# Kernel tuning notes

Measured on AMD Instinct MI355X. Metric: run time of the kernel, lower is better.

## Reference

```python
import jax, jax.numpy as jnp
import numpy as np

N, E = 50000, 800000
F_IN, F_OUT, H = 128, 16, 8
NEG_SLOPE = 0.2  # PyG GATConv default
EPS = 1e-5       # LayerNorm eps


def setup_inputs() -> dict:
    key = jax.random.key(0)
    ks = jax.random.split(key, 8)
    x = jax.random.normal(ks[0], (N, F_IN), dtype=jnp.float32)
    edge_index = jax.random.randint(ks[1], (2, E), 0, N, dtype=jnp.int32)
    s_in = 1.0 / np.sqrt(F_IN)
    s_f = 1.0 / np.sqrt(F_OUT)
    W = jax.random.normal(ks[2], (F_IN, H * F_OUT), dtype=jnp.float32) * s_in
    att_src = jax.random.normal(ks[3], (H, F_OUT), dtype=jnp.float32) * s_f
    att_dst = jax.random.normal(ks[4], (H, F_OUT), dtype=jnp.float32) * s_f
    bias = jnp.zeros((H * F_OUT,), dtype=jnp.float32)
    gamma = jnp.ones((H * F_OUT,), dtype=jnp.float32)
    beta = jnp.zeros((H * F_OUT,), dtype=jnp.float32)
    return {"x": x, "edge_index": edge_index, "W": W, "att_src": att_src,
            "att_dst": att_dst, "bias": bias, "gamma": gamma, "beta": beta}


def _gat_layer(x, edge_index, W, att_src, att_dst, bias, gamma, beta):
    n = x.shape[0]
    # add self loops (PyG GATConv default add_self_loops=True)
    loop = jnp.arange(n, dtype=edge_index.dtype)
    src = jnp.concatenate([edge_index[0], loop])  # message source j
    dst = jnp.concatenate([edge_index[1], loop])  # message target i

    xp = (x @ W).reshape(n, H, F_OUT)                      # [N,H,F]
    a_src = jnp.einsum('nhf,hf->nh', xp, att_src)          # [N,H]
    a_dst = jnp.einsum('nhf,hf->nh', xp, att_dst)          # [N,H]

    e = a_src[src] + a_dst[dst]                            # [E+N,H]
    e = jax.nn.leaky_relu(e, NEG_SLOPE)
    # softmax over incoming edges per destination node
    m = jax.ops.segment_max(e, dst, num_segments=n)        # [N,H]
    e = jnp.exp(e - m[dst])
    z = jax.ops.segment_sum(e, dst, num_segments=n)        # [N,H]
    alpha = e / jnp.where(z[dst] > 0, z[dst], 1.0)         # [E+N,H]

    msg = alpha[:, :, None] * xp[src]                      # [E+N,H,F]
    out = jax.ops.segment_sum(msg, dst, num_segments=n)    # [N,H,F]
    out = out.reshape(n, H * F_OUT) + bias

    # LayerNorm over feature dim
    mu = out.mean(axis=-1, keepdims=True)
    var = out.var(axis=-1, keepdims=True)
    return (out - mu) * jax.lax.rsqrt(var + EPS) * gamma + beta


def reference(x, edge_index, W, att_src, att_dst, bias, gamma, beta):
    return _gat_layer(x, edge_index, W, att_src, att_dst, bias, gamma, beta)
```

## Files before the change

### kernel.cpp

```cpp
#include <hip/hip_runtime.h>
#include <math.h>

#define F_IN 128
#define NHD 8
#define FEAT 128
#define NEG_SLOPE 0.2f
#define LN_EPS 1e-5f
#define BSH 7
#define BMSK 127
#define NPQ 16
#define CAP 48
#define EPB 4096
#define NBMAX 512
#define BCAP 6144
#define WCOLS 144

typedef __bf16 v8bf __attribute__((ext_vector_type(8)));
typedef __bf16 v4bf __attribute__((ext_vector_type(4)));
typedef __bf16 v2bf __attribute__((ext_vector_type(2)));
typedef float f32x4 __attribute__((ext_vector_type(4)));

__global__ __launch_bounds__(256) void k_wt(const float* __restrict__ W,
                                            const float* __restrict__ att_src,
                                            const float* __restrict__ att_dst,
                                            __bf16* __restrict__ WT,
                                            int* __restrict__ gcnt, int NB) {
    int idx = blockIdx.x * 256 + threadIdx.x;
    if (idx < NB) gcnt[idx] = 0;
    int c = idx >> 7, k = idx & 127;
    float v;
    if (c < 128) {
        v = W[k * 128 + c];
    } else if (c < 136) {
        int h = c - 128;
        float s = 0.f;
#pragma unroll
        for (int f = 0; f < 16; ++f) s += W[k * 128 + h * 16 + f] * att_src[h * 16 + f];
        v = s;
    } else {
        int h = c - 136;
        float s = 0.f;
#pragma unroll
        for (int f = 0; f < 16; ++f) s += W[k * 128 + h * 16 + f] * att_dst[h * 16 + f];
        v = s;
    }
    WT[c * 128 + k] = (__bf16)v;
}

__global__ __launch_bounds__(512) void k_fused(const float* __restrict__ x,
                                               const __bf16* __restrict__ WT,
                                               __bf16* __restrict__ xp16,
                                               float* __restrict__ a_src,
                                               float* __restrict__ a_dst,
                                               const int* __restrict__ src,
                                               const int* __restrict__ dst,
                                               unsigned int* __restrict__ sorted2,
                                               int* __restrict__ gcnt,
                                               int n, int E, int Ga) {
    __shared__ __align__(16) char smem[34816];
    if ((int)blockIdx.x < Ga) {
        unsigned int* sorted_l = (unsigned int*)smem;
        int* lcnt = (int*)(smem + 16384);
        int* loff = (int*)(smem + 16384 + 2048);
        int* wtot = (int*)(smem + 16384 + 2048 + 2052);
        int* wexcl = (int*)(smem + 16384 + 2048 + 2052 + 32);
        int* goff = (int*)(smem + 16384 + 2048 + 2052 + 64);
        int NB = (n + BMSK) >> BSH;
        int tid = threadIdx.x, lane = tid & 63, wid = tid >> 6;
        long base0 = (long)blockIdx.x * EPB;
        long total = (long)E + n;
        if (tid < NB) lcnt[tid] = 0;
        __syncthreads();

        int s0[8], d0[8];
        bool val[8];
        long e0 = base0 + (long)tid * 8;
        if (e0 + 7 < E) {
            int4 sa = *(const int4*)(src + e0);
            int4 sb = *(const int4*)(src + e0 + 4);
            int4 da = *(const int4*)(dst + e0);
            int4 db = *(const int4*)(dst + e0 + 4);
            s0[0] = sa.x; s0[1] = sa.y; s0[2] = sa.z; s0[3] = sa.w;
            s0[4] = sb.x; s0[5] = sb.y; s0[6] = sb.z; s0[7] = sb.w;
            d0[0] = da.x; d0[1] = da.y; d0[2] = da.z; d0[3] = da.w;
            d0[4] = db.x; d0[5] = db.y; d0[6] = db.z; d0[7] = db.w;
#pragma unroll
            for (int j = 0; j < 8; ++j) val[j] = true;
        } else {
#pragma unroll
            for (int j = 0; j < 8; ++j) {
                long e = e0 + j;
                val[j] = (e < total);
                s0[j] = d0[j] = 0;
                if (val[j]) {
                    if (e < E) { s0[j] = src[e]; d0[j] = dst[e]; }
                    else { s0[j] = d0[j] = (int)(e - E); }
                }
            }
        }
#pragma unroll
        for (int j = 0; j < 8; ++j)
            if (val[j]) atomicAdd(&lcnt[d0[j] >> BSH], 1);
        __syncthreads();

        int v = (tid < NB) ? lcnt[tid] : 0;
        int xx = v;
#pragma unroll
        for (int o = 1; o < 64; o <<= 1) {
            int t2 = __shfl_up(xx, o);
            if (lane >= o) xx += t2;
        }
        if (lane == 63) wtot[wid] = xx;
        __syncthreads();
        if (wid == 0 && lane < 8) {
            int s = wtot[lane];
            int y = s;
#pragma unroll
            for (int o = 1; o < 8; o <<= 1) {
                int t2 = __shfl_up(y, o);
                if (lane >= o) y += t2;
            }
            wexcl[lane] = y - s;
        }
        __syncthreads();
        int excl = wexcl[wid] + xx - v;
        if (tid < NB) loff[tid] = excl;
        if (tid == NB - 1) loff[NB] = excl + v;
        __syncthreads();
        if (tid < NB) lcnt[tid] = loff[tid];
        __syncthreads();
#pragma unroll
        for (int j = 0; j < 8; ++j) {
            if (val[j]) {
                int b = d0[j] >> BSH;
                int pos = atomicAdd(&lcnt[b], 1);
                sorted_l[pos] = ((unsigned)b << 23) | ((unsigned)s0[j] << 7) |
                                (unsigned)(d0[j] & BMSK);
            }
        }
        __syncthreads();
        if (tid < NB) {
            int len = loff[tid + 1] - loff[tid];
            goff[tid] = (len > 0) ? atomicAdd(&gcnt[tid], len) : 0;
        }
        __syncthreads();
        int tv = loff[NB];
        for (int i = tid; i < tv; i += 512) {
            unsigned int u = sorted_l[i];
            int b = (int)(u >> 23);
            int r = goff[b] + (i - loff[b]);
            if (r < BCAP)
                sorted2[(long)b * BCAP + r] = u & 0x7FFFFFu;
        }
    } else {
        __bf16 (*xs)[136] = (__bf16 (*)[136])smem;
        __bf16 (*ot)[136] = (__bf16 (*)[136])(smem + 17408);
        int gb = blockIdx.x - Ga;
        int tid = threadIdx.x;
        int rowbase = gb * 64;
        {
            int i4 = tid;
#pragma unroll
            for (int rep = 0; rep < 4; ++rep, i4 += 512) {
                int r = i4 >> 5, c4 = i4 & 31;
                int gr = rowbase + r; if (gr > n - 1) gr = n - 1;
                float4 xv = *(const float4*)(x + (long)gr * 128 + c4 * 4);
                v4bf pk;
                pk[0] = (__bf16)xv.x; pk[1] = (__bf16)xv.y;
                pk[2] = (__bf16)xv.z; pk[3] = (__bf16)xv.w;
                *(v4bf*)(&xs[r][c4 * 4]) = pk;
            }
        }
        __syncthreads();
        int wv = tid >> 6;
        int lane = tid & 63;
        int m = lane & 15, quad = lane >> 4;
        int colbase = wv * 16;
        const __bf16* wcol = WT + (colbase + m) * 128;
        v8bf wf[4];
#pragma unroll
        for (int kk = 0; kk < 4; ++kk)
            wf[kk] = *(const v8bf*)(wcol + kk * 32 + quad * 8);
        v8bf wf2[4];
        if (wv < 4) {
            const __bf16* wcol2 = WT + (128 + m) * 128;
#pragma unroll
            for (int kk = 0; kk < 4; ++kk)
                wf2[kk] = *(const v8bf*)(wcol2 + kk * 32 + quad * 8);
        }
#pragma unroll
        for (int t = 0; t < 4; ++t) {
            int rb = t * 16;
            f32x4 acc = {0.f, 0.f, 0.f, 0.f};
#pragma unroll
            for (int kk = 0; kk < 4; ++kk) {
                v8bf a = *(const v8bf*)(&xs[rb + m][kk * 32 + quad * 8]);
                acc = __builtin_amdgcn_mfma_f32_16x16x32_bf16(a, wf[kk], acc, 0, 0, 0);
            }
#pragma unroll
            for (int r = 0; r < 4; ++r)
                ot[rb + quad * 4 + r][colbase + m] = (__bf16)acc[r];
        }
        if (wv < 4) {
            int rb = wv * 16;
            f32x4 acc = {0.f, 0.f, 0.f, 0.f};
#pragma unroll
            for (int kk = 0; kk < 4; ++kk) {
                v8bf a = *(const v8bf*)(&xs[rb + m][kk * 32 + quad * 8]);
                acc = __builtin_amdgcn_mfma_f32_16x16x32_bf16(a, wf2[kk], acc, 0, 0, 0);
            }
#pragma unroll
            for (int r = 0; r < 4; ++r) {
                int row = rowbase + rb + quad * 4 + r;
                if (row < n) {
                    if (m < 8) a_src[row * 8 + m] = acc[r];
                    else       a_dst[row * 8 + (m - 8)] = acc[r];
                }
            }
        }
        __syncthreads();
        int r0 = tid >> 4, c8 = tid & 15;
#pragma unroll
        for (int pass = 0; pass < 2; ++pass) {
            int r = r0 + pass * 32;
            int gr = rowbase + r;
            if (gr < n) {
                v8bf vv = *(const v8bf*)(&ot[r][c8 * 8]);
                *(v8bf*)(xp16 + (long)gr * FEAT + c8 * 8) = vv;
            }
        }
    }
}

__global__ __launch_bounds__(256) void k_ba(const unsigned int* __restrict__ sorted2,
                                            const int* __restrict__ bcnt,
                                            const float* __restrict__ a_src,
                                            const float* __restrict__ a_dst,
                                            const __bf16* __restrict__ xp16,
                                            const float* __restrict__ bias,
                                            const float* __restrict__ gamma,
                                            const float* __restrict__ beta,
                                            const int* __restrict__ src,
                                            const int* __restrict__ dst,
                                            float* __restrict__ out, int n, int E) {
    __shared__ int slds[NPQ * CAP];
    __shared__ int lc[NPQ];
    __shared__ float adst_s[NPQ * NHD];
    int b = blockIdx.x >> 3;
    int q = blockIdx.x & 7;
    int tid = threadIdx.x;
    int node0 = (b << BSH) + q * NPQ;
    if (tid < NPQ) lc[tid] = 0;
    if (tid < NPQ * NHD) {
        int nd = node0 + (tid >> 3);
        adst_s[tid] = (nd < n) ? a_dst[nd * NHD + (tid & 7)] : 0.f;
    }
    __syncthreads();

    int cnt_b = bcnt[b]; if (cnt_b > BCAP) cnt_b = BCAP;
    const unsigned int* sg = sorted2 + (long)b * BCAP;
    int qlo = q * NPQ;
    for (int i = tid; i < cnt_b; i += 256) {
        unsigned int u = sg[i];
        int dl = (int)(u & BMSK) - qlo;
        if ((unsigned)dl < (unsigned)NPQ) {
            int p = atomicAdd(&lc[dl], 1);
            if (p < CAP) slds[dl * CAP + p] = (int)(u >> BSH);
        }
    }
    __syncthreads();
    if (tid < NPQ) {
        int cc = lc[tid]; if (cc > CAP) cc = CAP;
        int pad = (cc + 7) & ~7; if (pad > CAP) pad = CAP;
        for (int p = cc; p < pad; ++p) slds[tid * CAP + p] = 0;
    }
    __syncthreads();

    int lane = tid & 63, wv = tid >> 6;
    int h = lane & 7, j8 = lane >> 3;
    float2 bs = *(const float2*)(bias + 2 * lane);
    float2 g  = *(const float2*)(gamma + 2 * lane);
    float2 bt = *(const float2*)(beta + 2 * lane);

    for (int i = wv; i < NPQ; i += 4) {
        int node = node0 + i;
        if (node >= n) break;
        int cnt = lc[i];
        float acc0 = 0.f, acc1 = 0.f, inv;

        if (cnt <= CAP) {
            const int* row = slds + i * CAP;
            float b_h = adst_s[i * NHD + h];
            float zacc = 0.f;
            for (int base = 0; base < cnt; base += 8) {
                int s_my = row[base + j8];
                float e = a_src[s_my * NHD + h] + b_h;
                e = e > 0.f ? e : NEG_SLOPE * e;
                float w_my = (base + j8 < cnt) ? __expf(e) : 0.f;
                zacc += w_my;
                int ss[8];
#pragma unroll
                for (int j = 0; j < 8; ++j) ss[j] = row[base + j];
                float2 vals[8];
#pragma unroll
                for (int j = 0; j < 8; ++j) {
                    v2bf p = *(const v2bf*)(xp16 + (long)ss[j] * FEAT + 2 * lane);
                    vals[j] = make_float2((float)p[0], (float)p[1]);
                }
#pragma unroll
                for (int j = 0; j < 8; ++j) {
                    float w = __shfl(w_my, j * 8 + j8);
                    acc0 = fmaf(w, vals[j].x, acc0);
                    acc1 = fmaf(w, vals[j].y, acc1);
                }
            }
            zacc += __shfl_xor(zacc, 8);
            zacc += __shfl_xor(zacc, 16);
            zacc += __shfl_xor(zacc, 32);
            float z = __shfl(zacc, j8);
            inv = 1.f / z;
        } else {
            float b_h = a_dst[node * NHD + j8];
            float z = 0.f;
            {
                float e = a_src[node * NHD + j8] + b_h;
                e = e > 0.f ? e : NEG_SLOPE * e;
                float w = __expf(e);
                z += w;
                v2bf p = *(const v2bf*)(xp16 + (long)node * FEAT + 2 * lane);
                acc0 = fmaf(w, (float)p[0], acc0);
                acc1 = fmaf(w, (float)p[1], acc1);
            }
            for (int base = 0; base < E; base += 64) {
                int e = base + lane;
                int sv = 0;
                bool mt = false;
                if (e < E) { mt = (dst[e] == node); if (mt) sv = src[e]; }
                unsigned long long mask = __ballot(mt);
                while (mask) {
                    int bl = __ffsll(mask) - 1;
                    mask &= mask - 1;
                    int s = __shfl(sv, bl);
                    float ee = a_src[s * NHD + j8] + b_h;
                    ee = ee > 0.f ? ee : NEG_SLOPE * ee;
                    float w = __expf(ee);
                    z += w;
                    v2bf p = *(const v2bf*)(xp16 + (long)s * FEAT + 2 * lane);
                    acc0 = fmaf(w, (float)p[0], acc0);
                    acc1 = fmaf(w, (float)p[1], acc1);
                }
            }
            inv = 1.f / z;
        }

        float v0 = acc0 * inv + bs.x;
        float v1 = acc1 * inv + bs.y;
        float ssum = v0 + v1;
        float ssq = v0 * v0 + v1 * v1;
#pragma unroll
        for (int o = 32; o > 0; o >>= 1) {
            ssum += __shfl_xor(ssum, o);
            ssq += __shfl_xor(ssq, o);
        }
        float mu = ssum * (1.0f / FEAT);
        float var = ssq * (1.0f / FEAT) - mu * mu;
        float rs = rsqrtf(var + LN_EPS);
        float2 o2;
        o2.x = (v0 - mu) * rs * g.x + bt.x;
        o2.y = (v1 - mu) * rs * g.y + bt.y;
        *(float2*)(out + (long)node * FEAT + 2 * lane) = o2;
    }
}

extern "C" void kernel_launch(void* const* d_in, const int* in_sizes, int n_in,
                              void* d_out, int out_size, void* d_ws, size_t ws_size,
                              hipStream_t stream) {
    const float* x = (const float*)d_in[0];
    const int* edge_index = (const int*)d_in[1];
    const float* W = (const float*)d_in[2];
    const float* att_src = (const float*)d_in[3];
    const float* att_dst = (const float*)d_in[4];
    const float* bias = (const float*)d_in[5];
    const float* gamma = (const float*)d_in[6];
    const float* beta = (const float*)d_in[7];
    float* out = (float*)d_out;

    int n = in_sizes[0] / F_IN;
    int E = in_sizes[1] / 2;
    const int* src = edge_index;
    const int* dst = edge_index + E;
    int NB = (n + BMSK) >> BSH;
    int Ga = (E + n + EPB - 1) / EPB;
    int Gg = (n + 63) / 64;

    char* ws = (char*)d_ws;
    __bf16* WT   = (__bf16*)ws;                    ws += (size_t)WCOLS * 128 * 2;
    __bf16* xp16 = (__bf16*)ws;                    ws += (size_t)n * FEAT * 2;
    float* a_src = (float*)ws;                     ws += (size_t)n * NHD * 4;
    float* a_dst = (float*)ws;                     ws += (size_t)n * NHD * 4;
    unsigned int* sorted2 = (unsigned int*)ws;     ws += (size_t)NB * BCAP * 4;
    int* gcnt = (int*)ws;                          ws += (size_t)NB * 4;

    k_wt<<<72, 256, 0, stream>>>(W, att_src, att_dst, WT, gcnt, NB);
    k_fused<<<Ga + Gg, 512, 0, stream>>>(x, WT, xp16, a_src, a_dst,
                                         src, dst, sorted2, gcnt, n, E, Ga);
    k_ba<<<NB * 8, 256, 0, stream>>>(sorted2, gcnt, a_src, a_dst, xp16,
                                     bias, gamma, beta, src, dst, out, n, E);
}
```

Measured before the change: 149.9 us.

## Shard bucket lists per XCD and remap k_ba blocks for L2 locality

Splits each destination bucket's global edge list into 8 sub-lists keyed by blockIdx&7 (the XCD the writing block lands on), so global atomics and scattered writes stay within one XCD's L2. k_ba now assigns all 8 quarter-blocks of a bucket to the same XCD, so the repeated reads of that bucket's list hit that XCD's L2. The consumer then walks 8 sub-lists instead of one, and each sub-list has its own fixed capacity of 1024, which could overflow on skewed inputs where a single contiguous list would not.

```diff
diff --git a/kernel.cpp b/kernel.cpp
--- a/kernel.cpp
+++ b/kernel.cpp
@@ -12,7 +12,7 @@
 #define CAP 48
 #define EPB 4096
 #define NBMAX 512
-#define BCAP 6144
+#define SCAP 1024
 #define WCOLS 144
 
 typedef __bf16 v8bf __attribute__((ext_vector_type(8)));
@@ -26,7 +26,7 @@
                                             __bf16* __restrict__ WT,
                                             int* __restrict__ gcnt, int NB) {
     int idx = blockIdx.x * 256 + threadIdx.x;
-    if (idx < NB) gcnt[idx] = 0;
+    if (idx < NB * 8) gcnt[idx] = 0;
     int c = idx >> 7, k = idx & 127;
     float v;
     if (c < 128) {
@@ -66,6 +66,7 @@
         int* wexcl = (int*)(smem + 16384 + 2048 + 2052 + 32);
         int* goff = (int*)(smem + 16384 + 2048 + 2052 + 64);
         int NB = (n + BMSK) >> BSH;
+        int g = (int)(blockIdx.x & 7);
         int tid = threadIdx.x, lane = tid & 63, wid = tid >> 6;
         long base0 = (long)blockIdx.x * EPB;
         long total = (long)E + n;
@@ -141,7 +142,7 @@
         __syncthreads();
         if (tid < NB) {
             int len = loff[tid + 1] - loff[tid];
-            goff[tid] = (len > 0) ? atomicAdd(&gcnt[tid], len) : 0;
+            goff[tid] = (len > 0) ? atomicAdd(&gcnt[tid * 8 + g], len) : 0;
         }
         __syncthreads();
         int tv = loff[NB];
@@ -149,8 +150,8 @@
             unsigned int u = sorted_l[i];
             int b = (int)(u >> 23);
             int r = goff[b] + (i - loff[b]);
-            if (r < BCAP)
-                sorted2[(long)b * BCAP + r] = u & 0x7FFFFFu;
+            if (r < SCAP)
+                sorted2[((long)b * 8 + g) * SCAP + r] = u & 0x7FFFFFu;
         }
     } else {
         __bf16 (*xs)[136] = (__bf16 (*)[136])smem;
@@ -233,7 +234,7 @@
 }
 
 __global__ __launch_bounds__(256) void k_ba(const unsigned int* __restrict__ sorted2,
-                                            const int* __restrict__ bcnt,
+                                            const int* __restrict__ gcnt,
                                             const float* __restrict__ a_src,
                                             const float* __restrict__ a_dst,
                                             const __bf16* __restrict__ xp16,
@@ -242,12 +243,17 @@
                                             const float* __restrict__ beta,
                                             const int* __restrict__ src,
                                             const int* __restrict__ dst,
-                                            float* __restrict__ out, int n, int E) {
+                                            float* __restrict__ out, int n, int E,
+                                            int NB) {
+    int xcd = (int)(blockIdx.x & 7);
+    int slot = (int)(blockIdx.x >> 3);
+    int b = xcd + 8 * (slot >> 3);
+    int q = slot & 7;
+    if (b >= NB) return;
+
     __shared__ int slds[NPQ * CAP];
     __shared__ int lc[NPQ];
     __shared__ float adst_s[NPQ * NHD];
-    int b = blockIdx.x >> 3;
-    int q = blockIdx.x & 7;
     int tid = threadIdx.x;
     int node0 = (b << BSH) + q * NPQ;
     if (tid < NPQ) lc[tid] = 0;
@@ -257,15 +263,17 @@
     }
     __syncthreads();
 
-    int cnt_b = bcnt[b]; if (cnt_b > BCAP) cnt_b = BCAP;
-    const unsigned int* sg = sorted2 + (long)b * BCAP;
     int qlo = q * NPQ;
-    for (int i = tid; i < cnt_b; i += 256) {
-        unsigned int u = sg[i];
-        int dl = (int)(u & BMSK) - qlo;
-        if ((unsigned)dl < (unsigned)NPQ) {
-            int p = atomicAdd(&lc[dl], 1);
-            if (p < CAP) slds[dl * CAP + p] = (int)(u >> BSH);
+    for (int g = 0; g < 8; ++g) {
+        int cnt_g = gcnt[b * 8 + g]; if (cnt_g > SCAP) cnt_g = SCAP;
+        const unsigned int* sg = sorted2 + ((long)b * 8 + g) * SCAP;
+        for (int i = tid; i < cnt_g; i += 256) {
+            unsigned int u = sg[i];
+            int dl = (int)(u & BMSK) - qlo;
+            if ((unsigned)dl < (unsigned)NPQ) {
+                int p = atomicAdd(&lc[dl], 1);
+                if (p < CAP) slds[dl * CAP + p] = (int)(u >> BSH);
+            }
         }
     }
     __syncthreads();
@@ -279,7 +287,7 @@
     int lane = tid & 63, wv = tid >> 6;
     int h = lane & 7, j8 = lane >> 3;
     float2 bs = *(const float2*)(bias + 2 * lane);
-    float2 g  = *(const float2*)(gamma + 2 * lane);
+    float2 g2 = *(const float2*)(gamma + 2 * lane);
     float2 bt = *(const float2*)(beta + 2 * lane);
 
     for (int i = wv; i < NPQ; i += 4) {
@@ -366,8 +374,8 @@
         float var = ssq * (1.0f / FEAT) - mu * mu;
         float rs = rsqrtf(var + LN_EPS);
         float2 o2;
-        o2.x = (v0 - mu) * rs * g.x + bt.x;
-        o2.y = (v1 - mu) * rs * g.y + bt.y;
+        o2.x = (v0 - mu) * rs * g2.x + bt.x;
+        o2.y = (v1 - mu) * rs * g2.y + bt.y;
         *(float2*)(out + (long)node * FEAT + 2 * lane) = o2;
     }
 }
@@ -390,6 +398,7 @@
     const int* src = edge_index;
     const int* dst = edge_index + E;
     int NB = (n + BMSK) >> BSH;
+    int NB8 = (NB + 7) & ~7;
     int Ga = (E + n + EPB - 1) / EPB;
     int Gg = (n + 63) / 64;
 
@@ -398,12 +407,12 @@
     __bf16* xp16 = (__bf16*)ws;                    ws += (size_t)n * FEAT * 2;
     float* a_src = (float*)ws;                     ws += (size_t)n * NHD * 4;
     float* a_dst = (float*)ws;                     ws += (size_t)n * NHD * 4;
-    unsigned int* sorted2 = (unsigned int*)ws;     ws += (size_t)NB * BCAP * 4;
-    int* gcnt = (int*)ws;                          ws += (size_t)NB * 4;
+    unsigned int* sorted2 = (unsigned int*)ws;     ws += (size_t)NB * 8 * SCAP * 4;
+    int* gcnt = (int*)ws;                          ws += (size_t)NB * 8 * 4;
 
     k_wt<<<72, 256, 0, stream>>>(W, att_src, att_dst, WT, gcnt, NB);
     k_fused<<<Ga + Gg, 512, 0, stream>>>(x, WT, xp16, a_src, a_dst,
                                          src, dst, sorted2, gcnt, n, E, Ga);
-    k_ba<<<NB * 8, 256, 0, stream>>>(sorted2, gcnt, a_src, a_dst, xp16,
-                                     bias, gamma, beta, src, dst, out, n, E);
+    k_ba<<<NB8 * 8, 256, 0, stream>>>(sorted2, gcnt, a_src, a_dst, xp16,
+                                      bias, gamma, beta, src, dst, out, n, E, NB);
 }
```

Result: no change. 152.1 us (+1.5%).

## Replace bucketed two-level edge sort with per-node atomic adjacency lists

Applied to the files above, without the earlier changes.

Drops the block-local counting sort into 128-node buckets, which needed shared-memory scans, several barriers and a global bucket append. Each edge now does one global atomicAdd on a per-destination counter and writes its source into a fixed CAP-slot per-node list. The aggregation kernel then loads each node's list directly instead of rescanning its whole bucket and filtering by destination. The cost is heavy global atomic contention across 850k edges, a larger workspace of n*CAP ints, and uncoalesced scattered writes.

```diff
diff --git a/kernel.cpp b/kernel.cpp
--- a/kernel.cpp
+++ b/kernel.cpp
@@ -6,13 +6,9 @@
 #define FEAT 128
 #define NEG_SLOPE 0.2f
 #define LN_EPS 1e-5f
-#define BSH 7
-#define BMSK 127
 #define NPQ 16
 #define CAP 48
 #define EPB 4096
-#define NBMAX 512
-#define BCAP 6144
 #define WCOLS 144
 
 typedef __bf16 v8bf __attribute__((ext_vector_type(8)));
@@ -24,27 +20,29 @@
                                             const float* __restrict__ att_src,
                                             const float* __restrict__ att_dst,
                                             __bf16* __restrict__ WT,
-                                            int* __restrict__ gcnt, int NB) {
+                                            int* __restrict__ nodecnt, int n) {
     int idx = blockIdx.x * 256 + threadIdx.x;
-    if (idx < NB) gcnt[idx] = 0;
-    int c = idx >> 7, k = idx & 127;
-    float v;
-    if (c < 128) {
-        v = W[k * 128 + c];
-    } else if (c < 136) {
-        int h = c - 128;
-        float s = 0.f;
-#pragma unroll
-        for (int f = 0; f < 16; ++f) s += W[k * 128 + h * 16 + f] * att_src[h * 16 + f];
-        v = s;
-    } else {
-        int h = c - 136;
-        float s = 0.f;
-#pragma unroll
-        for (int f = 0; f < 16; ++f) s += W[k * 128 + h * 16 + f] * att_dst[h * 16 + f];
-        v = s;
-    }
-    WT[c * 128 + k] = (__bf16)v;
+    if (idx < n) nodecnt[idx] = 0;
+    if (idx < WCOLS * 128) {
+        int c = idx >> 7, k = idx & 127;
+        float v;
+        if (c < 128) {
+            v = W[k * 128 + c];
+        } else if (c < 136) {
+            int h = c - 128;
+            float s = 0.f;
+#pragma unroll
+            for (int f = 0; f < 16; ++f) s += W[k * 128 + h * 16 + f] * att_src[h * 16 + f];
+            v = s;
+        } else {
+            int h = c - 136;
+            float s = 0.f;
+#pragma unroll
+            for (int f = 0; f < 16; ++f) s += W[k * 128 + h * 16 + f] * att_dst[h * 16 + f];
+            v = s;
+        }
+        WT[c * 128 + k] = (__bf16)v;
+    }
 }
 
 __global__ __launch_bounds__(512) void k_fused(const float* __restrict__ x,
@@ -54,24 +52,13 @@
                                                float* __restrict__ a_dst,
                                                const int* __restrict__ src,
                                                const int* __restrict__ dst,
-                                               unsigned int* __restrict__ sorted2,
-                                               int* __restrict__ gcnt,
+                                               int* __restrict__ nodelist,
+                                               int* __restrict__ nodecnt,
                                                int n, int E, int Ga) {
-    __shared__ __align__(16) char smem[34816];
     if ((int)blockIdx.x < Ga) {
-        unsigned int* sorted_l = (unsigned int*)smem;
-        int* lcnt = (int*)(smem + 16384);
-        int* loff = (int*)(smem + 16384 + 2048);
-        int* wtot = (int*)(smem + 16384 + 2048 + 2052);
-        int* wexcl = (int*)(smem + 16384 + 2048 + 2052 + 32);
-        int* goff = (int*)(smem + 16384 + 2048 + 2052 + 64);
-        int NB = (n + BMSK) >> BSH;
-        int tid = threadIdx.x, lane = tid & 63, wid = tid >> 6;
+        int tid = threadIdx.x;
         long base0 = (long)blockIdx.x * EPB;
         long total = (long)E + n;
-        if (tid < NB) lcnt[tid] = 0;
-        __syncthreads();
-
         int s0[8], d0[8];
         bool val[8];
         long e0 = base0 + (long)tid * 8;
@@ -99,60 +86,15 @@
             }
         }
 #pragma unroll
-        for (int j = 0; j < 8; ++j)
-            if (val[j]) atomicAdd(&lcnt[d0[j] >> BSH], 1);
-        __syncthreads();
-
-        int v = (tid < NB) ? lcnt[tid] : 0;
-        int xx = v;
-#pragma unroll
-        for (int o = 1; o < 64; o <<= 1) {
-            int t2 = __shfl_up(xx, o);
-            if (lane >= o) xx += t2;
-        }
-        if (lane == 63) wtot[wid] = xx;
-        __syncthreads();
-        if (wid == 0 && lane < 8) {
-            int s = wtot[lane];
-            int y = s;
-#pragma unroll
-            for (int o = 1; o < 8; o <<= 1) {
-                int t2 = __shfl_up(y, o);
-                if (lane >= o) y += t2;
-            }
-            wexcl[lane] = y - s;
-        }
-        __syncthreads();
-        int excl = wexcl[wid] + xx - v;
-        if (tid < NB) loff[tid] = excl;
-        if (tid == NB - 1) loff[NB] = excl + v;
-        __syncthreads();
-        if (tid < NB) lcnt[tid] = loff[tid];
-        __syncthreads();
-#pragma unroll
         for (int j = 0; j < 8; ++j) {
             if (val[j]) {
-                int b = d0[j] >> BSH;
-                int pos = atomicAdd(&lcnt[b], 1);
-                sorted_l[pos] = ((unsigned)b << 23) | ((unsigned)s0[j] << 7) |
-                                (unsigned)(d0[j] & BMSK);
-            }
-        }
-        __syncthreads();
-        if (tid < NB) {
-            int len = loff[tid + 1] - loff[tid];
-            goff[tid] = (len > 0) ? atomicAdd(&gcnt[tid], len) : 0;
-        }
-        __syncthreads();
-        int tv = loff[NB];
-        for (int i = tid; i < tv; i += 512) {
-            unsigned int u = sorted_l[i];
-            int b = (int)(u >> 23);
-            int r = goff[b] + (i - loff[b]);
-            if (r < BCAP)
-                sorted2[(long)b * BCAP + r] = u & 0x7FFFFFu;
+                int pos = atomicAdd(&nodecnt[d0[j]], 1);
+                if (pos < CAP)
+                    nodelist[(long)d0[j] * CAP + pos] = s0[j];
+            }
         }
     } else {
+        __shared__ __align__(16) char smem[34816];
         __bf16 (*xs)[136] = (__bf16 (*)[136])smem;
         __bf16 (*ot)[136] = (__bf16 (*)[136])(smem + 17408);
         int gb = blockIdx.x - Ga;
@@ -232,8 +174,8 @@
     }
 }
 
-__global__ __launch_bounds__(256) void k_ba(const unsigned int* __restrict__ sorted2,
-                                            const int* __restrict__ bcnt,
+__global__ __launch_bounds__(256) void k_ba(const int* __restrict__ nodelist,
+                                            const int* __restrict__ nodecnt,
                                             const float* __restrict__ a_src,
                                             const float* __restrict__ a_dst,
                                             const __bf16* __restrict__ xp16,
@@ -246,27 +188,22 @@
     __shared__ int slds[NPQ * CAP];
     __shared__ int lc[NPQ];
     __shared__ float adst_s[NPQ * NHD];
-    int b = blockIdx.x >> 3;
-    int q = blockIdx.x & 7;
     int tid = threadIdx.x;
-    int node0 = (b << BSH) + q * NPQ;
-    if (tid < NPQ) lc[tid] = 0;
+    int node0 = (int)blockIdx.x * NPQ;
+    if (tid < NPQ) {
+        int nd = node0 + tid;
+        lc[tid] = (nd < n) ? nodecnt[nd] : 0;
+    }
     if (tid < NPQ * NHD) {
         int nd = node0 + (tid >> 3);
         adst_s[tid] = (nd < n) ? a_dst[nd * NHD + (tid & 7)] : 0.f;
     }
-    __syncthreads();
-
-    int cnt_b = bcnt[b]; if (cnt_b > BCAP) cnt_b = BCAP;
-    const unsigned int* sg = sorted2 + (long)b * BCAP;
-    int qlo = q * NPQ;
-    for (int i = tid; i < cnt_b; i += 256) {
-        unsigned int u = sg[i];
-        int dl = (int)(u & BMSK) - qlo;
-        if ((unsigned)dl < (unsigned)NPQ) {
-            int p = atomicAdd(&lc[dl], 1);
-            if (p < CAP) slds[dl * CAP + p] = (int)(u >> BSH);
-        }
+    long gbase = (long)node0 * CAP;
+    long glim = (long)n * CAP;
+#pragma unroll
+    for (int rep = 0; rep < 3; ++rep) {
+        int i = tid + rep * 256;
+        slds[i] = (gbase + i < glim) ? nodelist[gbase + i] : 0;
     }
     __syncthreads();
     if (tid < NPQ) {
@@ -389,21 +326,23 @@
     int E = in_sizes[1] / 2;
     const int* src = edge_index;
     const int* dst = edge_index + E;
-    int NB = (n + BMSK) >> BSH;
     int Ga = (E + n + EPB - 1) / EPB;
     int Gg = (n + 63) / 64;
+    int Gb = (n + NPQ - 1) / NPQ;
+    int wtotal = WCOLS * 128; if (n > wtotal) wtotal = n;
+    int Gw = (wtotal + 255) / 256;
 
     char* ws = (char*)d_ws;
     __bf16* WT   = (__bf16*)ws;                    ws += (size_t)WCOLS * 128 * 2;
     __bf16* xp16 = (__bf16*)ws;                    ws += (size_t)n * FEAT * 2;
     float* a_src = (float*)ws;                     ws += (size_t)n * NHD * 4;
     float* a_dst = (float*)ws;                     ws += (size_t)n * NHD * 4;
-    unsigned int* sorted2 = (unsigned int*)ws;     ws += (size_t)NB * BCAP * 4;
-    int* gcnt = (int*)ws;                          ws += (size_t)NB * 4;
-
-    k_wt<<<72, 256, 0, stream>>>(W, att_src, att_dst, WT, gcnt, NB);
+    int* nodelist = (int*)ws;                      ws += (size_t)n * CAP * 4;
+    int* nodecnt = (int*)ws;                       ws += (size_t)n * 4;
+
+    k_wt<<<Gw, 256, 0, stream>>>(W, att_src, att_dst, WT, nodecnt, n);
     k_fused<<<Ga + Gg, 512, 0, stream>>>(x, WT, xp16, a_src, a_dst,
-                                         src, dst, sorted2, gcnt, n, E, Ga);
-    k_ba<<<NB * 8, 256, 0, stream>>>(sorted2, gcnt, a_src, a_dst, xp16,
-                                     bias, gamma, beta, src, dst, out, n, E);
+                                         src, dst, nodelist, nodecnt, n, E, Ga);
+    k_ba<<<Gb, 256, 0, stream>>>(nodelist, nodecnt, a_src, a_dst, xp16,
+                                 bias, gamma, beta, src, dst, out, n, E);
 }
```

Measured after the change: 179.2 us. 19.5% more time.
